# Performance work log

Measured on AMD Instinct MI355X. Metric: run time of the kernel, lower is better.

Reference implementation:

```python
import jax, jax.numpy as jnp
import numpy as np

ROPE_BASE = 10000.0
CHUNK = 2048
NEG_INF = -1e30


def _rope(q, k, start_index):
    # q, k: (B, T, H, Dh) with Dh even; half-split RoPE as in RotaryEmbedding
    B, T, H, Dh = q.shape
    half = Dh // 2
    inv_freq = jnp.exp(jnp.arange(half, dtype=jnp.float32) * (-(np.log(ROPE_BASE) / half)))
    pos = jnp.arange(T, dtype=jnp.float32) + jnp.float32(start_index)
    ang = pos[:, None] * inv_freq[None, :]              # (T, half)
    cos = jnp.cos(ang)[None, :, None, :].astype(q.dtype)  # (1,T,1,half)
    sin = jnp.sin(ang)[None, :, None, :].astype(q.dtype)

    def rot(x):
        x1, x2 = x[..., :half], x[..., half:]
        return jnp.concatenate([x1 * cos - x2 * sin, x2 * cos + x1 * sin], axis=-1)

    return rot(q), rot(k)


def reference(q, k, v, start_index):
    # Chunked causal self-attention, softmax(QK^T) V with scale = 1.0 (Megalodon Eq. 9).
    B, T, H, Dh = q.shape
    Dv = v.shape[-1]
    q, k = _rope(q, k, start_index)

    nc = T // CHUNK  # T assumed multiple of chunk_size (prefill path, no cache)
    qc = q.reshape(B, nc, CHUNK, H, Dh)
    kc = k.reshape(B, nc, CHUNK, H, Dh)
    vc = v.reshape(B, nc, CHUNK, H, Dv)

    # per-chunk causal mask (C, C): 0 where j <= i else -inf
    i = jnp.arange(CHUNK)
    causal = (i[None, :] <= i[:, None])

    scores = jnp.einsum('bnqhd,bnkhd->bnhqk', qc, kc)  # scale = 1.0
    scores = jnp.where(causal[None, None, None, :, :], scores, NEG_INF)
    probs = jax.nn.softmax(scores, axis=-1)
    out = jnp.einsum('bnhqk,bnkhd->bnqhd', probs, vc)
    return out.reshape(B, T, H, Dv)


def setup_inputs() -> dict:
    key = jax.random.key(0)
    kq, kk, kv = jax.random.split(key, 3)
    B, T, H, Dh, Dv = 2, 4096, 16, 128, 128
    return {
        'q': jax.random.normal(kq, (B, T, H, Dh), dtype=jnp.float32),
        'k': jax.random.normal(kk, (B, T, H, Dh), dtype=jnp.float32),
        'v': jax.random.normal(kv, (B, T, H, Dv), dtype=jnp.float32),
        'start_index': 0,
    }
```

## Files before the change

### kernel.cpp

```cpp
#include <hip/hip_runtime.h>


#define T_TOT  4096
#define HH     16
#define DH     128
#define CHUNKL 2048
#define QT     128
#define KTILE  64
#define NEGV   1e30f
#define L2E    1.44269504088896f
#define THRL2  11.5415603f

typedef _Float16 f16;
typedef __attribute__((ext_vector_type(8)))  _Float16 f16x8;
typedef __attribute__((ext_vector_type(4)))  _Float16 f16x4;
typedef __attribute__((ext_vector_type(2)))  _Float16 f16x2;
typedef __attribute__((ext_vector_type(4)))  float    f32x4;
typedef __attribute__((ext_vector_type(16))) float    f32x16;
typedef __attribute__((ext_vector_type(4)))  int      i32x4;

#define AS_G(p) ((const __attribute__((address_space(1))) void*)(p))
#define AS_L(p) ((__attribute__((address_space(3))) void*)(p))

__device__ __forceinline__ f32x16 mfma32(f16x8 a, f16x8 b, f32x16 c) {
    return __builtin_amdgcn_mfma_f32_32x32x16_f16(a, b, c, 0, 0, 0);
}
__device__ __forceinline__ f32x4 mfma16(f16x8 a, f16x8 b, f32x4 c) {
    return __builtin_amdgcn_mfma_f32_16x16x32_f16(a, b, c, 0, 0, 0);
}
__device__ __forceinline__ int pk2(float a, float b) {
    f16x2 t; t[0] = (f16)a; t[1] = (f16)b;
    return __builtin_bit_cast(int, t);
}

__global__ void rope_table_kernel(float* __restrict__ tab, const int* __restrict__ startp) {
    int gid = blockIdx.x * blockDim.x + threadIdx.x;
    int t = gid >> 6, d = gid & 63;
    float pos  = (float)(t + *startp);
    float invf = expf((float)d * (-9.210340371976184f / 64.0f));
    float s, c;
    sincosf(pos * invf, &s, &c);
    tab[gid] = c;
    tab[T_TOT * 64 + gid] = s;
}

__global__ void prep_kv_kernel(const float* __restrict__ K, const float* __restrict__ V,
                               const float* __restrict__ tab,
                               f16* __restrict__ Kws, f16* __restrict__ VTws) {
    const int half = (2 * T_TOT * HH * DH) / 8;
    int gid = blockIdx.x * blockDim.x + threadIdx.x;
    if (gid < half) {
        const int tile = gid >> 10, idx = gid & 1023;
        const int key = idx >> 4, c8 = idx & 15;
        const int dsw0 = c8 << 3;
        const int sw   = (key & 7) << 3;
        const int d0   = dsw0 ^ sw;
        const int kt = tile & 31, h = (tile >> 5) & 15, n = (tile >> 9) & 1, b = tile >> 10;
        const int t  = n * CHUNKL + kt * KTILE + key;
        const float* kp = K + ((size_t)(b * T_TOT + t) * HH + h) * DH;
        const int dl = d0 & 63;
        f32x4 xm0 = *(const f32x4*)(kp + d0);
        f32x4 xm1 = *(const f32x4*)(kp + d0 + 4);
        f32x4 xo0 = *(const f32x4*)(kp + (d0 ^ 64));
        f32x4 xo1 = *(const f32x4*)(kp + (d0 ^ 64) + 4);
        f32x4 cc0 = *(const f32x4*)(tab + t * 64 + dl);
        f32x4 cc1 = *(const f32x4*)(tab + t * 64 + dl + 4);
        f32x4 ss0 = *(const f32x4*)(tab + T_TOT * 64 + t * 64 + dl);
        f32x4 ss1 = *(const f32x4*)(tab + T_TOT * 64 + t * 64 + dl + 4);
        const float sgn = (d0 < 64) ? -1.f : 1.f;
        f16x8 out;
#pragma unroll
        for (int j = 0; j < 4; ++j) {
            out[j]     = (f16)(xm0[j] * cc0[j] + sgn * xo0[j] * ss0[j]);
            out[4 + j] = (f16)(xm1[j] * cc1[j] + sgn * xo1[j] * ss1[j]);
        }
        *(f16x8*)&Kws[(size_t)tile * 8192 + key * DH + dsw0] = out;
    } else {
        const int oc = gid - half;
        const int tile = oc >> 10, idx = oc & 1023;
        const int d = idx >> 3, c8 = idx & 7;
        const int ksw0 = c8 << 3;
        const int sw   = (d & 7) << 3;
        const int key0 = ksw0 ^ sw;
        const int kt = tile & 31, h = (tile >> 5) & 15, n = (tile >> 9) & 1, b = tile >> 10;
        const int t0 = n * CHUNKL + kt * KTILE + key0;
        const float* vp = V + ((size_t)(b * T_TOT + t0) * HH + h) * DH + d;
        f16x8 out;
#pragma unroll
        for (int j = 0; j < 8; ++j)
            out[j] = (f16)vp[(size_t)j * (HH * DH)];
        *(f16x8*)&VTws[(size_t)tile * 8192 + d * KTILE + ksw0] = out;
    }
}

__global__ __launch_bounds__(512, 2)
void attn_fast_kernel(const float* __restrict__ Q, const f16* __restrict__ Kws,
                      const f16* __restrict__ VTws, const float* __restrict__ tab,
                      float* __restrict__ O)
{
    __shared__ f16 Kl[2][KTILE * DH];
    __shared__ f16 VTl[2][KTILE * DH];

    const int bid = blockIdx.x;
    const int sb  = (bid & 7) * 64 + (bid >> 3);
    const int pr  = sb & 7;
    const int bnh = sb >> 3;
    const int hd = bnh & 15, n = (bnh >> 4) & 1, b = bnh >> 5;
    const int qtA = pr, qtB = 15 - pr;

    const int tid = threadIdx.x;
    const int w   = tid >> 6;
    const int wq  = w & 3;
    const int l   = tid & 63;
    const int hl  = l >> 5;
    const int c31 = l & 31;

    const int qt_w = (w < 4) ? qtA : qtB;
    const int q0   = qt_w * QT;
    const size_t bh = (size_t)b * T_TOT * (HH * DH) + (size_t)hd * DH;
    const size_t tile0 = ((size_t)(((b * 2 + n) * 16 + hd) * 32)) * 8192;

    const int qr = q0 + wq * 32 + c31;
    const int tg = n * CHUNKL + qr;
    const float* qp = Q + bh + (size_t)tg * (HH * DH);

    f16x8 qf[8];
#pragma unroll
    for (int ks = 0; ks < 8; ++ks) {
        const int dbase = ks * 16 + 8 * hl;
        const int dl    = dbase & 63;
        f32x4 xa0 = *(const f32x4*)(qp + dbase);
        f32x4 xa1 = *(const f32x4*)(qp + dbase + 4);
        f32x4 xb0 = *(const f32x4*)(qp + (dbase ^ 64));
        f32x4 xb1 = *(const f32x4*)(qp + (dbase ^ 64) + 4);
        float cc[8], ss[8];
        *(f32x4*)&cc[0] = *(const f32x4*)(tab + tg * 64 + dl);
        *(f32x4*)&cc[4] = *(const f32x4*)(tab + tg * 64 + dl + 4);
        *(f32x4*)&ss[0] = *(const f32x4*)(tab + T_TOT * 64 + tg * 64 + dl);
        *(f32x4*)&ss[4] = *(const f32x4*)(tab + T_TOT * 64 + tg * 64 + dl + 4);
        const float sgn = (dbase < 64) ? -1.f : 1.f;
        float xa[8] = {xa0[0],xa0[1],xa0[2],xa0[3],xa1[0],xa1[1],xa1[2],xa1[3]};
        float xb[8] = {xb0[0],xb0[1],xb0[2],xb0[3],xb1[0],xb1[1],xb1[2],xb1[3]};
        f16x8 f;
#pragma unroll
        for (int j = 0; j < 8; ++j)
            f[j] = (f16)((xa[j] * cc[j] + sgn * xb[j] * ss[j]) * L2E);
        qf[ks] = f;
    }

    f32x16 o[4];
    float mrun = -NEGV, lrun = 0.f;
#pragma unroll
    for (int dt = 0; dt < 4; ++dt)
#pragma unroll
        for (int r = 0; r < 16; ++r) o[dt][r] = 0.f;

    const int nkt = 2 * qtB + 2;
    int cur = 0;

#pragma unroll
    for (int i = 0; i < 2; ++i) {
        const int off = (i * 8 + w) * 512;
        __builtin_amdgcn_global_load_lds(AS_G(Kws  + tile0 + off + l * 8), AS_L(&Kl[0][off]),  16, 0, 0);
        __builtin_amdgcn_global_load_lds(AS_G(VTws + tile0 + off + l * 8), AS_L(&VTl[0][off]), 16, 0, 0);
    }

    for (int kt = 0; kt < nkt; ++kt) {
        __syncthreads();

        if (kt + 1 < nkt) {
            const f16* ks_ = Kws  + tile0 + (size_t)(kt + 1) * 8192;
            const f16* vs_ = VTws + tile0 + (size_t)(kt + 1) * 8192;
            const int nb = cur ^ 1;
#pragma unroll
            for (int i = 0; i < 2; ++i) {
                const int off = (i * 8 + w) * 512;
                __builtin_amdgcn_global_load_lds(AS_G(ks_ + off + l * 8), AS_L(&Kl[nb][off]),  16, 0, 0);
                __builtin_amdgcn_global_load_lds(AS_G(vs_ + off + l * 8), AS_L(&VTl[nb][off]), 16, 0, 0);
            }
        }

        const bool active = (kt * KTILE) < (q0 + wq * 32 + 32);
        if (active) {
            const f16* Klc  = Kl[cur];
            const f16* VTlc = VTl[cur];

            f32x16 s[2];
#pragma unroll
            for (int ts = 0; ts < 2; ++ts)
#pragma unroll
                for (int r = 0; r < 16; ++r) s[ts][r] = 0.f;

            __builtin_amdgcn_s_setprio(1);
#pragma unroll
            for (int ts = 0; ts < 2; ++ts) {
                const int key = ts * 32 + c31;
                const int swk = (key & 7) << 3;
#pragma unroll
                for (int ks = 0; ks < 8; ++ks) {
                    f16x8 kf = *(const f16x8*)&Klc[key * DH + ((ks * 16 + 8 * hl) ^ swk)];
                    s[ts] = mfma32(kf, qf[ks], s[ts]);
                }
            }
            __builtin_amdgcn_s_setprio(0);

            if (kt >= 2 * qt_w) {
#pragma unroll
                for (int ts = 0; ts < 2; ++ts)
#pragma unroll
                    for (int r = 0; r < 16; ++r) {
                        const int key = kt * KTILE + ts * 32 + (r & 3) + 8 * (r >> 2) + 4 * hl;
                        if (key > qr) s[ts][r] = -NEGV;
                    }
            }

            float mx = s[0][0];
#pragma unroll
            for (int r = 1; r < 16; ++r) mx = fmaxf(mx, s[0][r]);
#pragma unroll
            for (int r = 0; r < 16; ++r) mx = fmaxf(mx, s[1][r]);
            mx = fmaxf(mx, __shfl_xor(mx, 32));

            if (__any(mx > mrun + THRL2)) {
                const float mn = fmaxf(mrun, mx);
                const float al = exp2f(mrun - mn);
                mrun = mn;
                lrun *= al;
#pragma unroll
                for (int dt = 0; dt < 4; ++dt)
#pragma unroll
                    for (int r = 0; r < 16; ++r) o[dt][r] *= al;
            }

            float ps = 0.f;
#pragma unroll
            for (int ts = 0; ts < 2; ++ts)
#pragma unroll
                for (int r = 0; r < 16; ++r) {
                    const float p = exp2f(s[ts][r] - mrun);
                    s[ts][r] = p;
                    ps += p;
                }
            lrun += ps;

            f16x8 pb[4];
#pragma unroll
            for (int ts = 0; ts < 2; ++ts) {
#pragma unroll
                for (int gs = 0; gs < 2; ++gs) {
                    const int G = 8 * gs;
                    const int A  = pk2(s[ts][G + 0], s[ts][G + 1]);
                    const int Bw = pk2(s[ts][G + 2], s[ts][G + 3]);
                    const int C  = pk2(s[ts][G + 4], s[ts][G + 5]);
                    const int Dw = pk2(s[ts][G + 6], s[ts][G + 7]);
                    const int Y1 = hl ? A : C;
                    const int Y2 = hl ? Bw : Dw;
                    const int r1 = __shfl_xor(Y1, 32);
                    const int r2 = __shfl_xor(Y2, 32);
                    i32x4 bi;
                    bi[0] = hl ? r1 : A;
                    bi[1] = hl ? r2 : Bw;
                    bi[2] = hl ? C  : r1;
                    bi[3] = hl ? Dw : r2;
                    pb[2 * ts + gs] = __builtin_bit_cast(f16x8, bi);
                }
            }

            __builtin_amdgcn_s_setprio(1);
#pragma unroll
            for (int dt = 0; dt < 4; ++dt) {
                const int d   = dt * 32 + c31;
                const int swv = (d & 7) << 3;
#pragma unroll
                for (int ks = 0; ks < 4; ++ks) {
                    f16x8 vf = *(const f16x8*)&VTlc[d * KTILE + ((ks * 16 + 8 * hl) ^ swv)];
                    o[dt] = mfma32(vf, pb[ks], o[dt]);
                }
            }
            __builtin_amdgcn_s_setprio(0);
        }
        cur ^= 1;
    }

    const float lt  = lrun + __shfl_xor(lrun, 32);
    const float inv = 1.0f / lt;
    float* op = O + bh + (size_t)tg * (HH * DH);
#pragma unroll
    for (int dt = 0; dt < 4; ++dt) {
#pragma unroll
        for (int dd = 0; dd < 4; ++dd) {
            f32x4 val;
#pragma unroll
            for (int c = 0; c < 4; ++c) val[c] = o[dt][4 * dd + c] * inv;
            *(f32x4*)&op[dt * 32 + dd * 8 + 4 * hl] = val;
        }
    }
}

__global__ __launch_bounds__(256, 2)
void attn_kernel(const float* __restrict__ Q, const float* __restrict__ K,
                 const float* __restrict__ V, const int* __restrict__ startp,
                 float* __restrict__ O)
{
    __shared__ f16 Kl[KTILE * DH];
    __shared__ f16 VTl[DH * KTILE];
    __shared__ f16 Pl[4][32 * 72];

    const int bid = blockIdx.x;
    const int qt  = 15 - (bid & 15);
    const int bnh = bid >> 4;
    const int h = bnh & 15, n = (bnh >> 4) & 1, b = bnh >> 5;

    const int tid  = threadIdx.x;
    const int w    = tid >> 6;
    const int lane = tid & 63;
    const int g    = lane >> 4, m = lane & 15;

    const int q0 = qt * QT;
    const size_t bh = (size_t)b * T_TOT * (HH * DH) + (size_t)h * DH;
    const int start = *startp;

    f16x8  qf[2][4];
    float  mrun[2][4], lrun[2][4];
    f32x4  o[2][8];
    const f32x4 ZERO4 = {0.f, 0.f, 0.f, 0.f};

#pragma unroll
    for (int rs = 0; rs < 2; ++rs) {
#pragma unroll
        for (int r = 0; r < 4; ++r) { mrun[rs][r] = -NEGV; lrun[rs][r] = 0.f; }
#pragma unroll
        for (int dt = 0; dt < 8; ++dt) o[rs][dt] = ZERO4;

        const int tg = n * CHUNKL + q0 + w * 32 + rs * 16 + m;
        const float* qp = Q + bh + (size_t)tg * (HH * DH);
#pragma unroll
        for (int kc = 0; kc < 4; ++kc) {
            const int dbase = kc * 32 + g * 8;
            const int dlo   = dbase & 63;
            f32x4 xa0 = *(const f32x4*)(qp + dbase);
            f32x4 xa1 = *(const f32x4*)(qp + dbase + 4);
            f32x4 xb0 = *(const f32x4*)(qp + (dbase ^ 64));
            f32x4 xb1 = *(const f32x4*)(qp + (dbase ^ 64) + 4);
            float cc[8], ss[8];
#pragma unroll
            for (int j = 0; j < 8; ++j) {
                float invf = expf((float)(dlo + j) * (-9.210340371976184f / 64.0f));
                sincosf((float)(tg + start) * invf, &ss[j], &cc[j]);
            }
            const float sgn = (dbase < 64) ? -1.f : 1.f;
            float xa[8] = {xa0[0],xa0[1],xa0[2],xa0[3],xa1[0],xa1[1],xa1[2],xa1[3]};
            float xb[8] = {xb0[0],xb0[1],xb0[2],xb0[3],xb1[0],xb1[1],xb1[2],xb1[3]};
            f16x8 f;
#pragma unroll
            for (int j = 0; j < 8; ++j) f[j] = (f16)(xa[j] * cc[j] + sgn * xb[j] * ss[j]);
            qf[rs][kc] = f;
        }
    }

    const int nkt = 2 * qt + 2;
    for (int kt = 0; kt < nkt; ++kt) {
        __syncthreads();
#pragma unroll
        for (int it = 0; it < 4; ++it) {
            const int tau = tid + 256 * it;
            const int row = tau >> 4;
            const int d0  = (tau & 15) << 2;
            const int tg  = n * CHUNKL + kt * KTILE + row;
            const float* kp = K + bh + (size_t)tg * (HH * DH);
            f32x4 xa = *(const f32x4*)(kp + d0);
            f32x4 xb = *(const f32x4*)(kp + d0 + 64);
            f32x4 cc, ss;
#pragma unroll
            for (int j = 0; j < 4; ++j) {
                float invf = expf((float)(d0 + j) * (-9.210340371976184f / 64.0f));
                float sv, cv;
                sincosf((float)(tg + start) * invf, &sv, &cv);
                cc[j] = cv; ss[j] = sv;
            }
            f16x4 oA, oB;
#pragma unroll
            for (int j = 0; j < 4; ++j) {
                oA[j] = (f16)(xa[j] * cc[j] - xb[j] * ss[j]);
                oB[j] = (f16)(xb[j] * cc[j] + xa[j] * ss[j]);
            }
            const int sw = (row & 7) << 3;
            *(f16x4*)&Kl[row * DH + (d0 ^ sw)]        = oA;
            *(f16x4*)&Kl[row * DH + ((d0 + 64) ^ sw)] = oB;
        }
#pragma unroll
        for (int it = 0; it < 8; ++it) {
            const int tau = tid + 256 * it;
            const int key = tau & 63;
            const int d0  = (tau >> 6) << 2;
            const int tg  = n * CHUNKL + kt * KTILE + key;
            f32x4 x = *(const f32x4*)(V + bh + (size_t)tg * (HH * DH) + d0);
#pragma unroll
            for (int j = 0; j < 4; ++j) {
                const int d = d0 + j;
                VTl[d * KTILE + (key ^ ((d & 7) << 3))] = (f16)x[j];
            }
        }
        __syncthreads();

        const bool active = (kt * KTILE) < (q0 + w * 32 + 32);
        if (active) {
            f32x4 sa[2][4];
#pragma unroll
            for (int rs = 0; rs < 2; ++rs)
#pragma unroll
                for (int nt = 0; nt < 4; ++nt) sa[rs][nt] = ZERO4;
#pragma unroll
            for (int nt = 0; nt < 4; ++nt) {
                const int key = nt * 16 + m;
                const int swk = (key & 7) << 3;
#pragma unroll
                for (int kc = 0; kc < 4; ++kc) {
                    f16x8 bf = *(const f16x8*)&Kl[key * DH + ((kc * 32 + g * 8) ^ swk)];
                    sa[0][nt] = mfma16(qf[0][kc], bf, sa[0][nt]);
                    sa[1][nt] = mfma16(qf[1][kc], bf, sa[1][nt]);
                }
            }
            const bool domask = (kt >= 2 * qt);
#pragma unroll
            for (int rs = 0; rs < 2; ++rs) {
                if (domask) {
#pragma unroll
                    for (int nt = 0; nt < 4; ++nt) {
                        const int key = kt * KTILE + nt * 16 + m;
#pragma unroll
                        for (int r = 0; r < 4; ++r) {
                            const int qr = q0 + w * 32 + rs * 16 + 4 * g + r;
                            if (key > qr) sa[rs][nt][r] = -NEGV;
                        }
                    }
                }
                float mx[4];
#pragma unroll
                for (int r = 0; r < 4; ++r)
                    mx[r] = fmaxf(fmaxf(sa[rs][0][r], sa[rs][1][r]),
                                  fmaxf(sa[rs][2][r], sa[rs][3][r]));
#pragma unroll
                for (int off = 1; off < 16; off <<= 1)
#pragma unroll
                    for (int r = 0; r < 4; ++r)
                        mx[r] = fmaxf(mx[r], __shfl_xor(mx[r], off));
                float al[4], ps[4];
#pragma unroll
                for (int r = 0; r < 4; ++r) {
                    const float mn = fmaxf(mrun[rs][r], mx[r]);
                    al[r] = exp2f((mrun[rs][r] - mn) * L2E);
                    mrun[rs][r] = mn;
                    ps[r] = 0.f;
                }
#pragma unroll
                for (int nt = 0; nt < 4; ++nt)
#pragma unroll
                    for (int r = 0; r < 4; ++r) {
                        const float p = exp2f((sa[rs][nt][r] - mrun[rs][r]) * L2E);
                        sa[rs][nt][r] = p;
                        ps[r] += p;
                    }
#pragma unroll
                for (int off = 1; off < 16; off <<= 1)
#pragma unroll
                    for (int r = 0; r < 4; ++r)
                        ps[r] += __shfl_xor(ps[r], off);
#pragma unroll
                for (int r = 0; r < 4; ++r)
                    lrun[rs][r] = lrun[rs][r] * al[r] + ps[r];
#pragma unroll
                for (int dt = 0; dt < 8; ++dt)
#pragma unroll
                    for (int r = 0; r < 4; ++r)
                        o[rs][dt][r] *= al[r];
#pragma unroll
                for (int nt = 0; nt < 4; ++nt)
#pragma unroll
                    for (int r = 0; r < 4; ++r)
                        Pl[w][(rs * 16 + 4 * g + r) * 72 + nt * 16 + m] = (f16)sa[rs][nt][r];
            }
            f16x8 pa[2][2];
#pragma unroll
            for (int rs = 0; rs < 2; ++rs)
#pragma unroll
                for (int kc = 0; kc < 2; ++kc)
                    pa[rs][kc] = *(const f16x8*)&Pl[w][(rs * 16 + m) * 72 + kc * 32 + g * 8];
#pragma unroll
            for (int dt = 0; dt < 8; ++dt) {
                const int d   = dt * 16 + m;
                const int swv = (d & 7) << 3;
#pragma unroll
                for (int kc = 0; kc < 2; ++kc) {
                    f16x8 vf = *(const f16x8*)&VTl[d * KTILE + ((kc * 32 + g * 8) ^ swv)];
                    o[0][dt] = mfma16(pa[0][kc], vf, o[0][dt]);
                    o[1][dt] = mfma16(pa[1][kc], vf, o[1][dt]);
                }
            }
        }
    }

#pragma unroll
    for (int rs = 0; rs < 2; ++rs) {
#pragma unroll
        for (int r = 0; r < 4; ++r) {
            const float inv = 1.0f / lrun[rs][r];
            const int tg = n * CHUNKL + q0 + w * 32 + rs * 16 + 4 * g + r;
            float* op = O + bh + (size_t)tg * (HH * DH);
#pragma unroll
            for (int dt = 0; dt < 8; ++dt)
                op[dt * 16 + m] = o[rs][dt][r] * inv;
        }
    }
}

extern "C" void kernel_launch(void* const* d_in, const int* in_sizes, int n_in,
                              void* d_out, int out_size, void* d_ws, size_t ws_size,
                              hipStream_t stream) {
    const float* q = (const float*)d_in[0];
    const float* k = (const float*)d_in[1];
    const float* v = (const float*)d_in[2];
    const int* start = (const int*)d_in[3];
    float* out = (float*)d_out;

    const size_t tab_elems = (size_t)2 * T_TOT * 64;
    const size_t kv_elems  = (size_t)2 * T_TOT * HH * DH;
    const size_t need = tab_elems * sizeof(float) + 2 * kv_elems * sizeof(f16);

    if (ws_size >= need) {
        float* tab = (float*)d_ws;
        f16* Kws  = (f16*)((char*)d_ws + tab_elems * sizeof(float));
        f16* VTws = Kws + kv_elems;
        rope_table_kernel<<<(T_TOT * 64) / 256, 256, 0, stream>>>(tab, start);
        prep_kv_kernel<<<(int)(2 * (kv_elems / 8) / 256), 256, 0, stream>>>(k, v, tab, Kws, VTws);
        attn_fast_kernel<<<512, 512, 0, stream>>>(q, Kws, VTws, tab, out);
    } else {
        attn_kernel<<<64 * 16, 256, 0, stream>>>(q, k, v, start, out);
    }
}
```

Measured before the change: 235.6 us.

## Double attention key tile to 128 and interleave P packing with PV MFMAs

Raises the key/value tile per pipeline stage from 64 to 128 keys. The K and transposed-V workspace layout and the prep kernel change to match, so the attention loop runs half as many iterations with half as many barriers. QK MFMAs are reordered to loop over the head dimension first, and the P shuffle/pack is now done per 32-key group, interleaved with the PV MFMAs. The cost is double the LDS footprint (128KB of double buffers per block), which likely cuts resident blocks per CU from two to one. The causal diagonal tile is also larger, so more masked work is wasted.

Result: faster. 220.8 us (-6.3%).

```diff
diff --git a/kernel.cpp b/kernel.cpp
--- a/kernel.cpp
+++ b/kernel.cpp
@@ -7,6 +7,7 @@
 #define CHUNKL 2048
 #define QT     128
 #define KTILE  64
+#define KTB    128
 #define NEGV   1e30f
 #define L2E    1.44269504088896f
 #define THRL2  11.5415603f
@@ -50,13 +51,13 @@
     const int half = (2 * T_TOT * HH * DH) / 8;
     int gid = blockIdx.x * blockDim.x + threadIdx.x;
     if (gid < half) {
-        const int tile = gid >> 10, idx = gid & 1023;
+        const int tile = gid >> 11, idx = gid & 2047;
         const int key = idx >> 4, c8 = idx & 15;
         const int dsw0 = c8 << 3;
         const int sw   = (key & 7) << 3;
         const int d0   = dsw0 ^ sw;
-        const int kt = tile & 31, h = (tile >> 5) & 15, n = (tile >> 9) & 1, b = tile >> 10;
-        const int t  = n * CHUNKL + kt * KTILE + key;
+        const int kt = tile & 15, h = (tile >> 4) & 15, n = (tile >> 8) & 1, b = tile >> 9;
+        const int t  = n * CHUNKL + kt * KTB + key;
         const float* kp = K + ((size_t)(b * T_TOT + t) * HH + h) * DH;
         const int dl = d0 & 63;
         f32x4 xm0 = *(const f32x4*)(kp + d0);
@@ -74,22 +75,22 @@
             out[j]     = (f16)(xm0[j] * cc0[j] + sgn * xo0[j] * ss0[j]);
             out[4 + j] = (f16)(xm1[j] * cc1[j] + sgn * xo1[j] * ss1[j]);
         }
-        *(f16x8*)&Kws[(size_t)tile * 8192 + key * DH + dsw0] = out;
+        *(f16x8*)&Kws[(size_t)tile * 16384 + key * DH + dsw0] = out;
     } else {
         const int oc = gid - half;
-        const int tile = oc >> 10, idx = oc & 1023;
-        const int d = idx >> 3, c8 = idx & 7;
+        const int tile = oc >> 11, idx = oc & 2047;
+        const int d = idx >> 4, c8 = idx & 15;
         const int ksw0 = c8 << 3;
         const int sw   = (d & 7) << 3;
         const int key0 = ksw0 ^ sw;
-        const int kt = tile & 31, h = (tile >> 5) & 15, n = (tile >> 9) & 1, b = tile >> 10;
-        const int t0 = n * CHUNKL + kt * KTILE + key0;
+        const int kt = tile & 15, h = (tile >> 4) & 15, n = (tile >> 8) & 1, b = tile >> 9;
+        const int t0 = n * CHUNKL + kt * KTB + key0;
         const float* vp = V + ((size_t)(b * T_TOT + t0) * HH + h) * DH + d;
         f16x8 out;
 #pragma unroll
         for (int j = 0; j < 8; ++j)
             out[j] = (f16)vp[(size_t)j * (HH * DH)];
-        *(f16x8*)&VTws[(size_t)tile * 8192 + d * KTILE + ksw0] = out;
+        *(f16x8*)&VTws[(size_t)tile * 16384 + d * KTB + ksw0] = out;
     }
 }
 
@@ -98,8 +99,8 @@
                       const f16* __restrict__ VTws, const float* __restrict__ tab,
                       float* __restrict__ O)
 {
-    __shared__ f16 Kl[2][KTILE * DH];
-    __shared__ f16 VTl[2][KTILE * DH];
+    __shared__ f16 Kl[2][KTB * DH];
+    __shared__ f16 VTl[2][KTB * DH];
 
     const int bid = blockIdx.x;
     const int sb  = (bid & 7) * 64 + (bid >> 3);
@@ -118,7 +119,7 @@
     const int qt_w = (w < 4) ? qtA : qtB;
     const int q0   = qt_w * QT;
     const size_t bh = (size_t)b * T_TOT * (HH * DH) + (size_t)hd * DH;
-    const size_t tile0 = ((size_t)(((b * 2 + n) * 16 + hd) * 32)) * 8192;
+    const size_t tile0 = (size_t)bnh * (16 * 16384);
 
     const int qr = q0 + wq * 32 + c31;
     const int tg = n * CHUNKL + qr;
@@ -155,11 +156,11 @@
 #pragma unroll
         for (int r = 0; r < 16; ++r) o[dt][r] = 0.f;
 
-    const int nkt = 2 * qtB + 2;
+    const int nkt = qtB + 1;
     int cur = 0;
 
 #pragma unroll
-    for (int i = 0; i < 2; ++i) {
+    for (int i = 0; i < 4; ++i) {
         const int off = (i * 8 + w) * 512;
         __builtin_amdgcn_global_load_lds(AS_G(Kws  + tile0 + off + l * 8), AS_L(&Kl[0][off]),  16, 0, 0);
         __builtin_amdgcn_global_load_lds(AS_G(VTws + tile0 + off + l * 8), AS_L(&VTl[0][off]), 16, 0, 0);
@@ -169,56 +170,56 @@
         __syncthreads();
 
         if (kt + 1 < nkt) {
-            const f16* ks_ = Kws  + tile0 + (size_t)(kt + 1) * 8192;
-            const f16* vs_ = VTws + tile0 + (size_t)(kt + 1) * 8192;
+            const f16* ks_ = Kws  + tile0 + (size_t)(kt + 1) * 16384;
+            const f16* vs_ = VTws + tile0 + (size_t)(kt + 1) * 16384;
             const int nb = cur ^ 1;
 #pragma unroll
-            for (int i = 0; i < 2; ++i) {
+            for (int i = 0; i < 4; ++i) {
                 const int off = (i * 8 + w) * 512;
                 __builtin_amdgcn_global_load_lds(AS_G(ks_ + off + l * 8), AS_L(&Kl[nb][off]),  16, 0, 0);
                 __builtin_amdgcn_global_load_lds(AS_G(vs_ + off + l * 8), AS_L(&VTl[nb][off]), 16, 0, 0);
             }
         }
 
-        const bool active = (kt * KTILE) < (q0 + wq * 32 + 32);
+        const bool active = (kt * KTB) < (q0 + wq * 32 + 32);
         if (active) {
             const f16* Klc  = Kl[cur];
             const f16* VTlc = VTl[cur];
 
-            f32x16 s[2];
-#pragma unroll
-            for (int ts = 0; ts < 2; ++ts)
+            f32x16 s[4];
+#pragma unroll
+            for (int ts = 0; ts < 4; ++ts)
 #pragma unroll
                 for (int r = 0; r < 16; ++r) s[ts][r] = 0.f;
 
             __builtin_amdgcn_s_setprio(1);
 #pragma unroll
-            for (int ts = 0; ts < 2; ++ts) {
-                const int key = ts * 32 + c31;
-                const int swk = (key & 7) << 3;
-#pragma unroll
-                for (int ks = 0; ks < 8; ++ks) {
+            for (int ks = 0; ks < 8; ++ks) {
+#pragma unroll
+                for (int ts = 0; ts < 4; ++ts) {
+                    const int key = ts * 32 + c31;
+                    const int swk = (key & 7) << 3;
                     f16x8 kf = *(const f16x8*)&Klc[key * DH + ((ks * 16 + 8 * hl) ^ swk)];
                     s[ts] = mfma32(kf, qf[ks], s[ts]);
                 }
             }
             __builtin_amdgcn_s_setprio(0);
 
-            if (kt >= 2 * qt_w) {
-#pragma unroll
-                for (int ts = 0; ts < 2; ++ts)
+            if (kt == qt_w) {
+#pragma unroll
+                for (int ts = 0; ts < 4; ++ts)
 #pragma unroll
                     for (int r = 0; r < 16; ++r) {
-                        const int key = kt * KTILE + ts * 32 + (r & 3) + 8 * (r >> 2) + 4 * hl;
+                        const int key = kt * KTB + ts * 32 + (r & 3) + 8 * (r >> 2) + 4 * hl;
                         if (key > qr) s[ts][r] = -NEGV;
                     }
             }
 
             float mx = s[0][0];
 #pragma unroll
-            for (int r = 1; r < 16; ++r) mx = fmaxf(mx, s[0][r]);
-#pragma unroll
-            for (int r = 0; r < 16; ++r) mx = fmaxf(mx, s[1][r]);
+            for (int ts = 0; ts < 4; ++ts)
+#pragma unroll
+                for (int r = 0; r < 16; ++r) mx = fmaxf(mx, s[ts][r]);
             mx = fmaxf(mx, __shfl_xor(mx, 32));
 
             if (__any(mx > mrun + THRL2)) {
@@ -234,7 +235,7 @@
 
             float ps = 0.f;
 #pragma unroll
-            for (int ts = 0; ts < 2; ++ts)
+            for (int ts = 0; ts < 4; ++ts)
 #pragma unroll
                 for (int r = 0; r < 16; ++r) {
                     const float p = exp2f(s[ts][r] - mrun);
@@ -243,9 +244,10 @@
                 }
             lrun += ps;
 
-            f16x8 pb[4];
-#pragma unroll
-            for (int ts = 0; ts < 2; ++ts) {
+            __builtin_amdgcn_s_setprio(1);
+#pragma unroll
+            for (int ts = 0; ts < 4; ++ts) {
+                f16x8 pbg[2];
 #pragma unroll
                 for (int gs = 0; gs < 2; ++gs) {
                     const int G = 8 * gs;
@@ -262,19 +264,16 @@
                     bi[1] = hl ? r2 : Bw;
                     bi[2] = hl ? C  : r1;
                     bi[3] = hl ? Dw : r2;
-                    pb[2 * ts + gs] = __builtin_bit_cast(f16x8, bi);
-                }
-            }
-
-            __builtin_amdgcn_s_setprio(1);
-#pragma unroll
-            for (int dt = 0; dt < 4; ++dt) {
-                const int d   = dt * 32 + c31;
-                const int swv = (d & 7) << 3;
-#pragma unroll
-                for (int ks = 0; ks < 4; ++ks) {
-                    f16x8 vf = *(const f16x8*)&VTlc[d * KTILE + ((ks * 16 + 8 * hl) ^ swv)];
-                    o[dt] = mfma32(vf, pb[ks], o[dt]);
+                    pbg[gs] = __builtin_bit_cast(f16x8, bi);
+                }
+#pragma unroll
+                for (int dt = 0; dt < 4; ++dt) {
+                    const int d   = dt * 32 + c31;
+                    const int swv = (d & 7) << 3;
+                    f16x8 vf0 = *(const f16x8*)&VTlc[d * KTB + (((2 * ts) * 16 + 8 * hl) ^ swv)];
+                    o[dt] = mfma32(vf0, pbg[0], o[dt]);
+                    f16x8 vf1 = *(const f16x8*)&VTlc[d * KTB + (((2 * ts + 1) * 16 + 8 * hl) ^ swv)];
+                    o[dt] = mfma32(vf1, pbg[1], o[dt]);
                 }
             }
             __builtin_amdgcn_s_setprio(0);
```
